# Optimization experiments

Hardware: AMD Instinct MI355X
Metric: run time of the kernel (lower is better)

## Reference

```python
import jax, jax.numpy as jnp
import numpy as np

B, IN, OUT = 8192, 4096, 4096


def setup_inputs() -> dict:
    key = jax.random.key(0)
    k_x, k_w, k_t, k_n = jax.random.split(key, 4)
    # int8 activations and weights (stored as int8; accumulated in int32)
    x = jax.random.randint(k_x, (B, IN), -128, 128, dtype=jnp.int32).astype(jnp.int8)
    W = jax.random.randint(k_w, (OUT, IN), -128, 128, dtype=jnp.int32).astype(jnp.int8)
    # per-channel BN fold: additive term t (int32) and negative bitshift n
    t = jax.random.randint(k_t, (OUT,), -(1 << 15), 1 << 15, dtype=jnp.int32)
    n = jax.random.randint(k_n, (OUT,), -9, -6, dtype=jnp.int32)  # shift right by 6..8
    act_min = jnp.full((OUT,), -128, dtype=jnp.int32)
    act_max = jnp.full((OUT,), 127, dtype=jnp.int32)
    return {"x": x, "W": W, "t": t, "n": n, "act_min": act_min, "act_max": act_max}


def reference(x, W, t, n, act_min, act_max):
    # int32-accumulate int8 GEMM: F.linear(x, W) -> [B, OUT]
    acc = jnp.matmul(x.astype(jnp.int32), W.astype(jnp.int32).T)
    acc = acc + t  # broadcast per-output-channel bias add
    acc = jnp.right_shift(acc, -n)  # arithmetic right shift requantization
    acc = jnp.clip(acc, act_min, act_max)
    # pure_positive is False (act_min < 0) -> cast to small signed type
    return acc.astype(jnp.int8)
```

## Files before the change

kernel.cpp:

```cpp
#include <hip/hip_runtime.h>
#include <stdint.h>


#define BDIM 8192
#define INDIM 4096
#define OUTDIM 4096

typedef __attribute__((ext_vector_type(4))) int I4;
typedef __attribute__((ext_vector_type(16))) int I16;

__global__ __launch_bounds__(256) void pack_lds(const int* __restrict__ x,
                                                const int* __restrict__ W,
                                                uint32_t* __restrict__ xp,
                                                uint32_t* __restrict__ wp) {
    __shared__ uint32_t sb[8192];
    const int tid = threadIdx.x;
    const int bid = blockIdx.x;
    const int* src;
    uint32_t* dst;
    if (bid < 1024) {
        const int m32 = bid >> 2, q = bid & 3;
        src = x + (size_t)m32 * 32 * INDIM + q * 1024;
        dst = xp + (size_t)m32 * 32768 + q * 8192;
    } else {
        const int v = bid - 1024;
        const int n32 = v >> 2, q = v & 3;
        src = W + (size_t)n32 * 32 * INDIM + q * 1024;
        dst = wp + (size_t)n32 * 32768 + q * 8192;
    }
    const int kb_l = tid >> 3;
    const int lane_hi = ((tid >> 2) & 1) << 5;
    const int bslot = tid & 3;
#pragma unroll 4
    for (int rr = 0; rr < 32; ++rr) {
        int4 a = *(const int4*)(src + (size_t)rr * INDIM + tid * 4);
        uint32_t v = ((uint32_t)a.x & 255u) | (((uint32_t)a.y & 255u) << 8)
                   | (((uint32_t)a.z & 255u) << 16) | (((uint32_t)a.w & 255u) << 24);
        uint32_t idx = (uint32_t)(kb_l * 256 + (rr + lane_hi) * 4 + bslot);
        idx ^= ((idx >> 8) & 7u) << 2;
        sb[idx] = v;
    }
    __syncthreads();
#pragma unroll
    for (int it = 0; it < 8; ++it) {
        uint32_t idx = (uint32_t)(it * 1024 + tid * 4);
        idx ^= ((idx >> 8) & 7u) << 2;
        uint4 vv = *(const uint4*)&sb[idx];
        *(uint4*)(dst + it * 1024 + tid * 4) = vv;
    }
}

__device__ __forceinline__ void glds16(const void* g, void* l) {
    __builtin_amdgcn_global_load_lds((__attribute__((address_space(1))) void*)g,
                                     (__attribute__((address_space(3))) void*)l,
                                     16, 0, 0);
}

#define VMW4() asm volatile("s_waitcnt vmcnt(4)" ::: "memory")
#define VMW2() asm volatile("s_waitcnt vmcnt(2)" ::: "memory")
#define VMW0() asm volatile("s_waitcnt vmcnt(0)" ::: "memory")
#define BARRIER()                          \
    do {                                   \
        __builtin_amdgcn_s_barrier();      \
        asm volatile("" ::: "memory");     \
    } while (0)
#define SCHEDB() __builtin_amdgcn_sched_barrier(0)

#define STAGE(SETK, BUF)                                                          \
    do {                                                                          \
        _Pragma("unroll")                                                         \
        for (int i_ = 0; i_ < 2; ++i_)                                            \
            glds16(gsrc[i_] + (size_t)(SETK) * 1024,                              \
                   lds_raw + (BUF) * 16384 + (w * 2 + i_) * 1024);                \
    } while (0)

#define FRAG_READ(FA, FB, BUF)                                                    \
    do {                                                                          \
        const uint8_t* lb_ = lds_raw + (BUF) * 16384 + lane * 16;                 \
        _Pragma("unroll")                                                         \
        for (int i_ = 0; i_ < 4; ++i_)                                            \
            FA[i_] = *(const I4*)(lb_ + (wr4 + i_) * 1024);                       \
        _Pragma("unroll")                                                         \
        for (int j_ = 0; j_ < 2; ++j_)                                            \
            FB[j_] = *(const I4*)(lb_ + 8192 + (wc2 + j_) * 1024);                \
    } while (0)

#define MFMA_SET(FA, FB)                                                          \
    do {                                                                          \
        __builtin_amdgcn_s_setprio(1);                                            \
        _Pragma("unroll")                                                         \
        for (int i_ = 0; i_ < 4; ++i_)                                            \
            _Pragma("unroll")                                                     \
            for (int j_ = 0; j_ < 2; ++j_)                                        \
                acc[i_][j_] = __builtin_amdgcn_mfma_i32_32x32x32_i8(              \
                    FA[i_], FB[j_], acc[i_][j_], 0, 0, 0);                        \
        __builtin_amdgcn_s_setprio(0);                                            \
    } while (0)

__global__ __launch_bounds__(512, 2) void gemm_lds(
    const uint8_t* __restrict__ Xp,
    const uint8_t* __restrict__ Wp,
    const int* __restrict__ t, const int* __restrict__ nsh,
    const int* __restrict__ amin, const int* __restrict__ amax,
    int* __restrict__ out) {

    const int bn = blockIdx.x;
    const int bm = blockIdx.y;
    const int tid = threadIdx.x;
    const int lane = tid & 63;
    const int w = tid >> 6;
    const int wr = w >> 2;
    const int wc = w & 3;
    const int wr4 = wr * 4;
    const int wc2 = wc * 2;

    __shared__ uint8_t lds_raw[65536];

    const uint8_t* gsrc[2];
#pragma unroll
    for (int i = 0; i < 2; ++i) {
        const int s = w * 2 + i;
        gsrc[i] = (s < 8) ? Xp + ((size_t)(bm * 8 + s) << 17) + lane * 16
                          : Wp + ((size_t)(bn * 8 + (s - 8)) << 17) + lane * 16;
    }

    I16 acc[4][2];
#pragma unroll
    for (int i = 0; i < 4; ++i)
#pragma unroll
        for (int j = 0; j < 2; ++j)
#pragma unroll
            for (int r = 0; r < 16; ++r) acc[i][j][r] = 0;

    I4 a0[4], b0[2], a1[4], b1[2];

    STAGE(0, 0);
    STAGE(1, 1);
    STAGE(2, 2);
    VMW4();
    BARRIER();
    FRAG_READ(a0, b0, 0);

#pragma unroll 1
    for (int kk = 0; kk < 124; kk += 4) {
        VMW2(); BARRIER();
        STAGE(kk + 3, 3);
        FRAG_READ(a1, b1, 1);
        MFMA_SET(a0, b0);
        SCHEDB();
        VMW2(); BARRIER();
        STAGE(kk + 4, 0);
        FRAG_READ(a0, b0, 2);
        MFMA_SET(a1, b1);
        SCHEDB();
        VMW2(); BARRIER();
        STAGE(kk + 5, 1);
        FRAG_READ(a1, b1, 3);
        MFMA_SET(a0, b0);
        SCHEDB();
        VMW2(); BARRIER();
        STAGE(kk + 6, 2);
        FRAG_READ(a0, b0, 0);
        MFMA_SET(a1, b1);
        SCHEDB();
    }
    VMW2(); BARRIER();
    STAGE(127, 3);
    FRAG_READ(a1, b1, 1);
    MFMA_SET(a0, b0);
    SCHEDB();
    VMW2(); BARRIER();
    FRAG_READ(a0, b0, 2);
    MFMA_SET(a1, b1);
    SCHEDB();
    VMW0(); BARRIER();
    FRAG_READ(a1, b1, 3);
    MFMA_SET(a0, b0);
    SCHEDB();
    MFMA_SET(a1, b1);

#pragma unroll
    for (int j = 0; j < 2; ++j) {
        const int o = bn * 256 + wc2 * 32 + j * 32 + (lane & 31);
        const int tt = t[o];
        const int sh = -nsh[o];
        const int mn = amin[o];
        const int mx = amax[o];
#pragma unroll
        for (int i = 0; i < 4; ++i) {
            const int rowbase = bm * 256 + wr4 * 32 + i * 32 + 4 * (lane >> 5);
#pragma unroll
            for (int r = 0; r < 16; ++r) {
                const int row = rowbase + (r & 3) + 8 * (r >> 2);
                int v = acc[i][j][r] + tt;
                v >>= sh;
                v = v < mn ? mn : (v > mx ? mx : v);
                __builtin_nontemporal_store(v, &out[(size_t)row * OUTDIM + o]);
            }
        }
    }
}

extern "C" void kernel_launch(void* const* d_in, const int* in_sizes, int n_in,
                              void* d_out, int out_size, void* d_ws, size_t ws_size,
                              hipStream_t stream) {
    const int* x = (const int*)d_in[0];
    const int* W = (const int*)d_in[1];
    const int* t = (const int*)d_in[2];
    const int* n = (const int*)d_in[3];
    const int* amin = (const int*)d_in[4];
    const int* amax = (const int*)d_in[5];
    int* out = (int*)d_out;

    uint8_t* xp = (uint8_t*)d_ws;
    uint8_t* wp = xp + (size_t)BDIM * INDIM;

    pack_lds<<<1536, 256, 0, stream>>>(x, W, (uint32_t*)xp, (uint32_t*)wp);

    dim3 grid(OUTDIM / 256, BDIM / 256);
    gemm_lds<<<grid, 512, 0, stream>>>(xp, wp, t, n, amin, amax, out);
}
```

Before: 389.8 us.

## Restructure GEMM main loop into single-fragment phases with two barriers each

Replaces the ping-pong register double-buffered fragment pipeline with a per-phase schedule. Each phase reads fragments from LDS, issues the next global-to-LDS stage, hits a barrier, waits on lgkmcnt, then runs the MFMAs, and waits on vmcnt plus a second barrier. This halves fragment register usage and aligns waves (ping-pong style) so LDS reads and MFMA bursts of different waves interleave. It risks exposing LDS read latency before each MFMA set and adds one extra barrier per k-step.

```diff
diff --git a/kernel.cpp b/kernel.cpp
--- a/kernel.cpp
+++ b/kernel.cpp
@@ -59,6 +59,7 @@
 #define VMW4() asm volatile("s_waitcnt vmcnt(4)" ::: "memory")
 #define VMW2() asm volatile("s_waitcnt vmcnt(2)" ::: "memory")
 #define VMW0() asm volatile("s_waitcnt vmcnt(0)" ::: "memory")
+#define LGKM0() asm volatile("s_waitcnt lgkmcnt(0)" ::: "memory")
 #define BARRIER()                          \
     do {                                   \
         __builtin_amdgcn_s_barrier();      \
@@ -95,6 +96,31 @@
                 acc[i_][j_] = __builtin_amdgcn_mfma_i32_32x32x32_i8(              \
                     FA[i_], FB[j_], acc[i_][j_], 0, 0, 0);                        \
         __builtin_amdgcn_s_setprio(0);                                            \
+    } while (0)
+
+#define PHASE_S(KSET, BUF, SBUF, VMW_STMT)                                        \
+    do {                                                                          \
+        FRAG_READ(af, bf, BUF);                                                   \
+        STAGE((KSET) + 3, SBUF);                                                  \
+        BARRIER();                                                                \
+        LGKM0();                                                                  \
+        SCHEDB();                                                                 \
+        MFMA_SET(af, bf);                                                         \
+        SCHEDB();                                                                 \
+        VMW_STMT;                                                                 \
+        BARRIER();                                                                \
+    } while (0)
+
+#define PHASE_N(BUF, VMW_STMT)                                                    \
+    do {                                                                          \
+        FRAG_READ(af, bf, BUF);                                                   \
+        BARRIER();                                                                \
+        LGKM0();                                                                  \
+        SCHEDB();                                                                 \
+        MFMA_SET(af, bf);                                                         \
+        SCHEDB();                                                                 \
+        VMW_STMT;                                                                 \
+        BARRIER();                                                                \
     } while (0)
 
 __global__ __launch_bounds__(512, 2) void gemm_lds(
@@ -132,52 +158,28 @@
 #pragma unroll
             for (int r = 0; r < 16; ++r) acc[i][j][r] = 0;
 
-    I4 a0[4], b0[2], a1[4], b1[2];
+    I4 af[4], bf[2];
 
     STAGE(0, 0);
     STAGE(1, 1);
     STAGE(2, 2);
     VMW4();
     BARRIER();
-    FRAG_READ(a0, b0, 0);
 
 #pragma unroll 1
     for (int kk = 0; kk < 124; kk += 4) {
-        VMW2(); BARRIER();
-        STAGE(kk + 3, 3);
-        FRAG_READ(a1, b1, 1);
-        MFMA_SET(a0, b0);
-        SCHEDB();
-        VMW2(); BARRIER();
-        STAGE(kk + 4, 0);
-        FRAG_READ(a0, b0, 2);
-        MFMA_SET(a1, b1);
-        SCHEDB();
-        VMW2(); BARRIER();
-        STAGE(kk + 5, 1);
-        FRAG_READ(a1, b1, 3);
-        MFMA_SET(a0, b0);
-        SCHEDB();
-        VMW2(); BARRIER();
-        STAGE(kk + 6, 2);
-        FRAG_READ(a0, b0, 0);
-        MFMA_SET(a1, b1);
-        SCHEDB();
-    }
-    VMW2(); BARRIER();
-    STAGE(127, 3);
-    FRAG_READ(a1, b1, 1);
-    MFMA_SET(a0, b0);
+        PHASE_S(kk + 0, 0, 3, VMW4());
+        PHASE_S(kk + 1, 1, 0, VMW4());
+        PHASE_S(kk + 2, 2, 1, VMW4());
+        PHASE_S(kk + 3, 3, 2, VMW4());
+    }
+    PHASE_S(124, 0, 3, VMW4());
+    PHASE_N(1, VMW2());
+    PHASE_N(2, VMW0());
+    FRAG_READ(af, bf, 3);
+    LGKM0();
     SCHEDB();
-    VMW2(); BARRIER();
-    FRAG_READ(a0, b0, 2);
-    MFMA_SET(a1, b1);
-    SCHEDB();
-    VMW0(); BARRIER();
-    FRAG_READ(a1, b1, 3);
-    MFMA_SET(a0, b0);
-    SCHEDB();
-    MFMA_SET(a1, b1);
+    MFMA_SET(af, bf);
 
 #pragma unroll
     for (int j = 0; j < 2; ++j) {
```

After: 393.9 us. Within noise of the previous version (+1.0%).
